# Performance work log

Hardware: AMD Instinct MI355X
Metric: run time of the kernel (lower is better)

Reference implementation:

```python
import jax, jax.numpy as jnp
import numpy as np

B, N, D, U = 8, 4096, 128, 1024


def setup_inputs() -> dict:
    key = jax.random.key(0)
    kx, kw = jax.random.split(key)
    x = jax.random.normal(kx, (B, N, D), dtype=jnp.float32)
    # learned kernel, shape (dims, units) as in build()
    w = jax.random.normal(kw, (D, U), dtype=jnp.float32)
    return {"x": x, "w": w}


def reference(x, w):
    # Squared Euclidean distance from every point x[b,n,:] to every prototype
    # column w[:,u]: sum_d (x[b,n,d] - w[d,u])^2.
    # work is a single GEMM instead of materializing a [B,N,D,U] tensor.
    x2 = jnp.sum(x * x, axis=-1, keepdims=True)        # [B, N, 1]
    w2 = jnp.sum(w * w, axis=0)                        # [U]
    xw = jnp.einsum("bnd,du->bnu", x, w)               # [B, N, U]
    a = x2 + w2 - 2.0 * xw                             # [B, N, U]
    # inverted=False, activation=None -> return raw squared distances
    return a
```

## Files before the change

### kernel.cpp

```cpp
#include <hip/hip_runtime.h>

#define M_TOT 32768
#define K_DIM 128
#define U_TOT 1024

#define BM 128
#define BN 128
#define BK 32

typedef short s16x8 __attribute__((ext_vector_type(8)));
typedef float f32x4 __attribute__((ext_vector_type(4)));

__device__ inline unsigned int f2bf(float f) {
    union { float f; unsigned int u; } v; v.f = f;
    unsigned int r = v.u + 0x7FFFu + ((v.u >> 16) & 1u);
    return r >> 16;
}

__device__ inline void async_load16(const void* g, void* l) {
    __builtin_amdgcn_global_load_lds((const __attribute__((address_space(1))) void*)g,
                                     (__attribute__((address_space(3))) void*)l,
                                     16, 0, 0);
}

__global__ __launch_bounds__(256) void prep_kernel(
    const float* __restrict__ x, const float* __restrict__ w,
    unsigned int* __restrict__ xb, unsigned int* __restrict__ wt,
    float* __restrict__ x2, float* __restrict__ w2)
{
    const int lane = threadIdx.x & 63;
    const int gw = (blockIdx.x << 2) + (threadIdx.x >> 6);
    if (gw < M_TOT) {
        const float2 v = ((const float2*)(x + (size_t)gw * K_DIM))[lane];
        float s = v.x * v.x + v.y * v.y;
        #pragma unroll
        for (int off = 32; off; off >>= 1) s += __shfl_xor(s, off);
        xb[gw * 64 + lane] = f2bf(v.x) | (f2bf(v.y) << 16);
        if (lane == 0) x2[gw] = s;
    } else if (gw < M_TOT + U_TOT) {
        const int u = gw - M_TOT;
        const float a = w[(size_t)(2 * lane) * U_TOT + u];
        const float b = w[(size_t)(2 * lane + 1) * U_TOT + u];
        float s = a * a + b * b;
        #pragma unroll
        for (int off = 32; off; off >>= 1) s += __shfl_xor(s, off);
        wt[u * 64 + lane] = f2bf(a) | (f2bf(b) << 16);
        if (lane == 0) w2[u] = s;
    }
}

__global__ __launch_bounds__(256) void gemm_kernel(
    const unsigned short* __restrict__ xb, const unsigned short* __restrict__ wt,
    const float* __restrict__ x2, const float* __restrict__ w2,
    float* __restrict__ out)
{
    __shared__ __align__(16) unsigned short As[BM * BK];
    __shared__ __align__(16) unsigned short Bs[BN * BK];

    const int tid = threadIdx.x;
    const int wv = tid >> 6;
    const int lane = tid & 63;
    const int m0 = (int)(blockIdx.x >> 3) * BM;
    const int u0 = (int)(blockIdx.x & 7) * BN;
    const int wm = (wv & 1) * 64;
    const int wn = (wv >> 1) * 64;
    const int col = lane & 15;
    const int quad = lane >> 4;
    const int srow = lane >> 2;
    const int sch = (lane & 3) * 8;

    f32x4 acc[4][4] = {};

    #pragma unroll
    for (int kt = 0; kt < 4; ++kt) {
        const int k0 = kt * BK;
        #pragma unroll
        for (int i = 0; i < 2; ++i) {
            const int rb = (wv * 2 + i) * 16;
            async_load16(xb + (size_t)(m0 + rb + srow) * K_DIM + k0 + sch, &As[rb * BK]);
            async_load16(wt + (size_t)(u0 + rb + srow) * K_DIM + k0 + sch, &Bs[rb * BK]);
        }
        __syncthreads();

        s16x8 af[4], bfr[4];
        #pragma unroll
        for (int t = 0; t < 4; ++t) {
            af[t]  = *(const s16x8*)&As[(wm + t * 16 + col) * BK + quad * 8];
            bfr[t] = *(const s16x8*)&Bs[(wn + t * 16 + col) * BK + quad * 8];
        }
        #pragma unroll
        for (int a = 0; a < 4; ++a)
            #pragma unroll
            for (int b = 0; b < 4; ++b)
                acc[a][b] = __builtin_amdgcn_mfma_f32_16x16x32_bf16(af[a], bfr[b], acc[a][b], 0, 0, 0);
        __syncthreads();
    }

    const int orow = quad * 4;
    #pragma unroll
    for (int a = 0; a < 4; ++a) {
        const int mb = m0 + wm + a * 16 + orow;
        float xs[4];
        #pragma unroll
        for (int r = 0; r < 4; ++r) xs[r] = x2[mb + r];
        #pragma unroll
        for (int b = 0; b < 4; ++b) {
            const int u = u0 + wn + b * 16 + col;
            const float wsq = w2[u];
            float* op = out + (size_t)mb * U_TOT + u;
            #pragma unroll
            for (int r = 0; r < 4; ++r)
                op[(size_t)r * U_TOT] = xs[r] + wsq - 2.0f * acc[a][b][r];
        }
    }
}

__global__ __launch_bounds__(256) void fallback_kernel(
    const float* __restrict__ x, const float* __restrict__ w,
    float* __restrict__ out)
{
    __shared__ float xrow[K_DIM];
    const int m = blockIdx.x;
    const int tid = threadIdx.x;
    if (tid < K_DIM) xrow[tid] = x[(size_t)m * K_DIM + tid];
    __syncthreads();
    float x2 = 0.f;
    #pragma unroll
    for (int k = 0; k < K_DIM; ++k) x2 += xrow[k] * xrow[k];
    #pragma unroll
    for (int uu = 0; uu < 4; ++uu) {
        const int u = uu * 256 + tid;
        float dot = 0.f, w2 = 0.f;
        for (int k = 0; k < K_DIM; ++k) {
            const float wv = w[(size_t)k * U_TOT + u];
            dot += xrow[k] * wv;
            w2 += wv * wv;
        }
        out[(size_t)m * U_TOT + u] = x2 + w2 - 2.0f * dot;
    }
}

extern "C" void kernel_launch(void* const* d_in, const int* in_sizes, int n_in,
                              void* d_out, int out_size, void* d_ws, size_t ws_size,
                              hipStream_t stream) {
    const float* x = (const float*)d_in[0];
    const float* w = (const float*)d_in[1];
    float* out = (float*)d_out;

    const size_t need = (size_t)M_TOT * K_DIM * 2 + (size_t)U_TOT * K_DIM * 2
                      + (size_t)M_TOT * 4 + (size_t)U_TOT * 4;
    if (ws_size < need) {
        fallback_kernel<<<M_TOT, 256, 0, stream>>>(x, w, out);
        return;
    }

    unsigned short* xb = (unsigned short*)d_ws;
    unsigned short* wt = xb + (size_t)M_TOT * K_DIM;
    float* x2 = (float*)(wt + (size_t)U_TOT * K_DIM);
    float* w2 = x2 + M_TOT;

    prep_kernel<<<(M_TOT + U_TOT) / 4, 256, 0, stream>>>(x, w, (unsigned int*)xb,
                                                         (unsigned int*)wt, x2, w2);
    gemm_kernel<<<(M_TOT / BM) * (U_TOT / BN), 256, 0, stream>>>(xb, wt, x2, w2, out);
}
```

Before: 160.4 us.

## Restructure GEMM into persistent B-resident tiles with double-buffered A and 32x32 MFMA

The GEMM kernel now loads a 128-column slice of W once into LDS and keeps its fragments in registers. It then streams eight 64-row A tiles through double-buffered, XOR-swizzled LDS with full K=128 per tile, using 32x32x16 bf16 MFMA and 512-thread blocks with a remapped block order. The prep kernel also switches to float4 loads, processing two rows per wavefront. The aim is to cut redundant W loads, LDS bank conflicts and sync overhead, and to overlap loads with compute. The cost is fewer blocks (512) and higher register and LDS pressure.

Result: faster. 152.4 us (-5.0%).

```diff
diff --git a/kernel.cpp b/kernel.cpp
--- a/kernel.cpp
+++ b/kernel.cpp
@@ -4,17 +4,16 @@
 #define K_DIM 128
 #define U_TOT 1024
 
-#define BM 128
-#define BN 128
-#define BK 32
+#define GBM 64
+#define GBN 128
+#define NMS 8
 
 typedef short s16x8 __attribute__((ext_vector_type(8)));
-typedef float f32x4 __attribute__((ext_vector_type(4)));
+typedef float f32x16 __attribute__((ext_vector_type(16)));
 
 __device__ inline unsigned int f2bf(float f) {
     union { float f; unsigned int u; } v; v.f = f;
-    unsigned int r = v.u + 0x7FFFu + ((v.u >> 16) & 1u);
-    return r >> 16;
+    return (v.u + 0x7FFFu + ((v.u >> 16) & 1u)) >> 16;
 }
 
 __device__ inline void async_load16(const void* g, void* l) {
@@ -29,16 +28,21 @@
     float* __restrict__ x2, float* __restrict__ w2)
 {
     const int lane = threadIdx.x & 63;
-    const int gw = (blockIdx.x << 2) + (threadIdx.x >> 6);
-    if (gw < M_TOT) {
-        const float2 v = ((const float2*)(x + (size_t)gw * K_DIM))[lane];
-        float s = v.x * v.x + v.y * v.y;
+    const int lc = lane & 31;
+    if (blockIdx.x < 4096) {
+        const int wv = threadIdx.x >> 6;
+        const int row = (blockIdx.x << 3) + (wv << 1) + (lane >> 5);
+        const float4 v = ((const float4*)(x + (size_t)row * K_DIM))[lc];
+        float s = v.x * v.x + v.y * v.y + v.z * v.z + v.w * v.w;
         #pragma unroll
-        for (int off = 32; off; off >>= 1) s += __shfl_xor(s, off);
-        xb[gw * 64 + lane] = f2bf(v.x) | (f2bf(v.y) << 16);
-        if (lane == 0) x2[gw] = s;
-    } else if (gw < M_TOT + U_TOT) {
-        const int u = gw - M_TOT;
+        for (int off = 16; off; off >>= 1) s += __shfl_xor(s, off);
+        uint2 pk;
+        pk.x = f2bf(v.x) | (f2bf(v.y) << 16);
+        pk.y = f2bf(v.z) | (f2bf(v.w) << 16);
+        ((uint2*)xb)[(size_t)row * 32 + lc] = pk;
+        if (lc == 0) x2[row] = s;
+    } else {
+        const int u = ((blockIdx.x - 4096) << 2) + (threadIdx.x >> 6);
         const float a = w[(size_t)(2 * lane) * U_TOT + u];
         const float b = w[(size_t)(2 * lane + 1) * U_TOT + u];
         float s = a * a + b * b;
@@ -49,69 +53,88 @@
     }
 }
 
-__global__ __launch_bounds__(256) void gemm_kernel(
+__global__ __launch_bounds__(512, 4) void gemm_kernel(
     const unsigned short* __restrict__ xb, const unsigned short* __restrict__ wt,
     const float* __restrict__ x2, const float* __restrict__ w2,
     float* __restrict__ out)
 {
-    __shared__ __align__(16) unsigned short As[BM * BK];
-    __shared__ __align__(16) unsigned short Bs[BN * BK];
+    __shared__ __align__(16) unsigned short Bs[GBN * K_DIM];
+    __shared__ __align__(16) unsigned short As[2][GBM * K_DIM];
 
     const int tid = threadIdx.x;
     const int wv = tid >> 6;
     const int lane = tid & 63;
-    const int m0 = (int)(blockIdx.x >> 3) * BM;
-    const int u0 = (int)(blockIdx.x & 7) * BN;
-    const int wm = (wv & 1) * 64;
-    const int wn = (wv >> 1) * 64;
-    const int col = lane & 15;
-    const int quad = lane >> 4;
-    const int srow = lane >> 2;
-    const int sch = (lane & 3) * 8;
+    const int lc = lane & 31;
+    const int hi = lane >> 5;
 
-    f32x4 acc[4][4] = {};
+    const int b = blockIdx.x;
+    const int ut = (b >> 3) & 7;
+    const int msb = (b & 7) * 8 + (b >> 6);
+    const int u0 = ut * GBN;
+    const int mbase = msb * (GBM * NMS);
 
     #pragma unroll
-    for (int kt = 0; kt < 4; ++kt) {
-        const int k0 = kt * BK;
-        #pragma unroll
-        for (int i = 0; i < 2; ++i) {
-            const int rb = (wv * 2 + i) * 16;
-            async_load16(xb + (size_t)(m0 + rb + srow) * K_DIM + k0 + sch, &As[rb * BK]);
-            async_load16(wt + (size_t)(u0 + rb + srow) * K_DIM + k0 + sch, &Bs[rb * BK]);
-        }
-        __syncthreads();
-
-        s16x8 af[4], bfr[4];
-        #pragma unroll
-        for (int t = 0; t < 4; ++t) {
-            af[t]  = *(const s16x8*)&As[(wm + t * 16 + col) * BK + quad * 8];
-            bfr[t] = *(const s16x8*)&Bs[(wn + t * 16 + col) * BK + quad * 8];
-        }
-        #pragma unroll
-        for (int a = 0; a < 4; ++a)
-            #pragma unroll
-            for (int b = 0; b < 4; ++b)
-                acc[a][b] = __builtin_amdgcn_mfma_f32_16x16x32_bf16(af[a], bfr[b], acc[a][b], 0, 0, 0);
-        __syncthreads();
+    for (int i = 0; i < 4; ++i) {
+        const int p = (wv * 4 + i) * 64 + lane;
+        const int row = p >> 4;
+        const int j = (p & 15) ^ (row & 15);
+        async_load16(wt + ((size_t)(u0 + row) << 7) + j * 8, &Bs[(p & ~63) * 8]);
+    }
+    #pragma unroll
+    for (int i = 0; i < 2; ++i) {
+        const int p = (wv * 2 + i) * 64 + lane;
+        const int row = p >> 4;
+        const int j = (p & 15) ^ (row & 15);
+        async_load16(xb + ((size_t)(mbase + row) << 7) + j * 8, &As[0][(p & ~63) * 8]);
     }
 
-    const int orow = quad * 4;
+    const int wr = wv >> 2;
+    const int wc = wv & 3;
+    const float w2v = w2[u0 + wc * 32 + lc];
+
+    __syncthreads();
+
+    s16x8 bfrag[8];
     #pragma unroll
-    for (int a = 0; a < 4; ++a) {
-        const int mb = m0 + wm + a * 16 + orow;
-        float xs[4];
+    for (int st = 0; st < 8; ++st) {
+        const int row = wc * 32 + lc;
+        const int j0 = (st << 1) + hi;
+        bfrag[st] = *(const s16x8*)&Bs[((row << 4) + (j0 ^ (row & 15))) * 8];
+    }
+
+    #pragma unroll
+    for (int ms = 0; ms < NMS; ++ms) {
+        if (ms + 1 < NMS) {
+            #pragma unroll
+            for (int i = 0; i < 2; ++i) {
+                const int p = (wv * 2 + i) * 64 + lane;
+                const int row = p >> 4;
+                const int j = (p & 15) ^ (row & 15);
+                async_load16(xb + ((size_t)(mbase + (ms + 1) * GBM + row) << 7) + j * 8,
+                             &As[(ms + 1) & 1][(p & ~63) * 8]);
+            }
+        }
+
+        const int mb = mbase + ms * GBM + wr * 32;
+        const float x2row = x2[mb + lc];
+
+        f32x16 acc = {};
         #pragma unroll
-        for (int r = 0; r < 4; ++r) xs[r] = x2[mb + r];
+        for (int st = 0; st < 8; ++st) {
+            const int row = wr * 32 + lc;
+            const int j0 = (st << 1) + hi;
+            const s16x8 af = *(const s16x8*)&As[ms & 1][((row << 4) + (j0 ^ (row & 15))) * 8];
+            acc = __builtin_amdgcn_mfma_f32_32x32x16_bf16(af, bfrag[st], acc, 0, 0, 0);
+        }
+
+        float* op = out + (size_t)mb * U_TOT + u0 + wc * 32 + lc;
         #pragma unroll
-        for (int b = 0; b < 4; ++b) {
-            const int u = u0 + wn + b * 16 + col;
-            const float wsq = w2[u];
-            float* op = out + (size_t)mb * U_TOT + u;
-            #pragma unroll
-            for (int r = 0; r < 4; ++r)
-                op[(size_t)r * U_TOT] = xs[r] + wsq - 2.0f * acc[a][b][r];
+        for (int r = 0; r < 16; ++r) {
+            const int t = (r & 3) + ((r >> 2) << 3);
+            const float xs = __shfl(x2row, t + (hi << 2) + (lane & 32));
+            op[(size_t)(t + (hi << 2)) * U_TOT] = xs + w2v - 2.0f * acc[r];
         }
+        if (ms + 1 < NMS) __syncthreads();
     }
 }
 
@@ -159,7 +182,7 @@
     float* x2 = (float*)(wt + (size_t)U_TOT * K_DIM);
     float* w2 = x2 + M_TOT;
 
-    prep_kernel<<<(M_TOT + U_TOT) / 4, 256, 0, stream>>>(x, w, (unsigned int*)xb,
-                                                         (unsigned int*)wt, x2, w2);
-    gemm_kernel<<<(M_TOT / BM) * (U_TOT / BN), 256, 0, stream>>>(xb, wt, x2, w2, out);
+    prep_kernel<<<4096 + 256, 256, 0, stream>>>(x, w, (unsigned int*)xb,
+                                                (unsigned int*)wt, x2, w2);
+    gemm_kernel<<<(M_TOT / (GBM * NMS)) * (U_TOT / GBN), 512, 0, stream>>>(xb, wt, x2, w2, out);
 }
```
